# Kernel tuning notes

Hardware: AMD Instinct MI355X
Metric: run time of the kernel (lower is better)

## Reference

```python
import jax, jax.numpy as jnp
import numpy as np

B, T, C, H = 8, 2048, 1024, 128  # batch, seq (== block_size), n_embd, head_size


def setup_inputs() -> dict:
    key = jax.random.key(0)
    ks = jax.random.split(key, 4)
    s = 1.0 / np.sqrt(C)  # keep logits sane for softmax
    return {
        "embedded_data": jax.random.normal(ks[0], (B, T, C), dtype=jnp.float32),
        "Wq": jax.random.normal(ks[1], (C, H), dtype=jnp.float32) * s,
        "bq": jnp.zeros((H,), dtype=jnp.float32),
        "Wk": jax.random.normal(ks[2], (C, H), dtype=jnp.float32) * s,
        "bk": jnp.zeros((H,), dtype=jnp.float32),
        "Wv": jax.random.normal(ks[3], (C, H), dtype=jnp.float32) * s,
        "bv": jnp.zeros((H,), dtype=jnp.float32),
    }


def reference(embedded_data, Wq, bq, Wk, bk, Wv, bv):
    Bc, Tc, Cc = embedded_data.shape
    q = embedded_data @ Wq + bq                      # [B,T,H]
    k = embedded_data @ Wk + bk                      # [B,T,H]
    v = embedded_data @ Wv + bv                      # [B,T,H]
    # NOTE: source scales by C**-0.5 (input embed dim), not head_size**-0.5
    wei = jnp.einsum("bqh,bkh->bqk", q, k) * (Cc ** -0.5)  # [B,T,T]
    causal = jnp.tril(jnp.ones((Tc, Tc), dtype=bool))
    wei = jnp.where(causal, wei, -jnp.inf)
    wei = jax.nn.softmax(wei, axis=-1)
    # dropout(p=0.2) is identity in eval mode
    out = jnp.einsum("bqk,bkh->bqh", wei, v)         # [B,T,H]
    return out
```

## Files before the change

### kernel.cpp

```cpp
#include <hip/hip_runtime.h>
#include <cstdint>
#include <cstddef>

typedef __bf16 bf16x8 __attribute__((ext_vector_type(8)));
typedef float f32x4 __attribute__((ext_vector_type(4)));

#define B_ 8
#define T_ 2048
#define C_ 1024
#define H_ 128

#define QSC 0.045084220027780106f

__device__ __forceinline__ unsigned short f2bf(float f) {
    __bf16 h = (__bf16)f;
    return *(unsigned short*)&h;
}
__device__ __forceinline__ float bf2f(unsigned short u) {
    union { unsigned int i; float f; } x; x.i = ((unsigned int)u) << 16;
    return x.f;
}

__device__ __forceinline__ void gload16(void* lds, const void* g) {
    __builtin_amdgcn_global_load_lds(
        (const __attribute__((address_space(1))) unsigned int*)g,
        (__attribute__((address_space(3))) unsigned int*)lds, 16, 0, 0);
}

__global__ __launch_bounds__(256) void prep_w(
    const float* __restrict__ Wq, const float* __restrict__ Wk,
    const float* __restrict__ Wv, unsigned short* __restrict__ wt)
{
    int gid = blockIdx.x * 256 + threadIdx.x;
    int which = gid >> 14;
    int rem = gid & 16383;
    int n = rem >> 7;
    int kc = rem & 127;
    const float* W = which == 0 ? Wq : (which == 1 ? Wk : Wv);
    unsigned short tmp[8];
    #pragma unroll
    for (int i = 0; i < 8; ++i) tmp[i] = f2bf(W[(size_t)(kc * 8 + i) * H_ + n]);
    *(uint4*)&wt[((size_t)which * H_ + n) * C_ + kc * 8] = *(uint4*)tmp;
}

__global__ __launch_bounds__(384, 2) void proj_fused2(
    const float* __restrict__ x, const unsigned short* __restrict__ wt,
    const float* __restrict__ bq, const float* __restrict__ bk,
    const float* __restrict__ bv,
    unsigned short* __restrict__ qo, unsigned short* __restrict__ ko,
    unsigned short* __restrict__ vo)
{
    __shared__ float xs[2][64 * 64];
    __shared__ unsigned short ws2[2][384 * 64];

    const int tid = threadIdx.x;
    const int w = tid >> 6, l = tid & 63, gl = l >> 4, lc = l & 15;
    const int cb = w * 64;
    const int m0 = blockIdx.x * 64;

    f32x4 acc[4][4];
    #pragma unroll
    for (int im = 0; im < 4; ++im)
        #pragma unroll
        for (int jn = 0; jn < 4; ++jn) acc[im][jn] = f32x4{0.f, 0.f, 0.f, 0.f};

    auto stage = [&](int buf, int kc2) {
        const int kb = kc2 * 64;
        if (w < 4) {
            #pragma unroll
            for (int ji = 0; ji < 4; ++ji) {
                int slot = ji * 256 + tid;
                int r = slot >> 4, cs = slot & 15;
                gload16(&xs[buf][(ji * 256 + w * 64) * 4],
                        &x[(size_t)(m0 + r) * C_ + kb + ((cs ^ (r & 15)) * 4)]);
            }
        }
        #pragma unroll
        for (int ji = 0; ji < 8; ++ji) {
            int slot = ji * 384 + tid;
            int R = slot >> 3, cs = slot & 7;
            gload16(&ws2[buf][(ji * 384 + w * 64) * 8],
                    &wt[(size_t)R * C_ + kb + ((cs ^ (R & 7)) * 8)]);
        }
    };

    stage(0, 0);
    __syncthreads();

    int cur = 0;
    for (int kc = 0; kc < 16; ++kc) {
        if (kc < 15) stage(cur ^ 1, kc + 1);
        #pragma unroll
        for (int ks = 0; ks < 2; ++ks) {
            bf16x8 a[4], b[4];
            const int u0 = ks * 8 + gl * 2;
            #pragma unroll
            for (int im = 0; im < 4; ++im) {
                int row = im * 16 + lc;
                f32x4 lo = *(const f32x4*)&xs[cur][(row * 16 + (u0 ^ (row & 15))) * 4];
                f32x4 hi = *(const f32x4*)&xs[cur][(row * 16 + ((u0 + 1) ^ (row & 15))) * 4];
                bf16x8 af;
                af[0] = (__bf16)lo[0]; af[1] = (__bf16)lo[1];
                af[2] = (__bf16)lo[2]; af[3] = (__bf16)lo[3];
                af[4] = (__bf16)hi[0]; af[5] = (__bf16)hi[1];
                af[6] = (__bf16)hi[2]; af[7] = (__bf16)hi[3];
                a[im] = af;
            }
            #pragma unroll
            for (int jn = 0; jn < 4; ++jn) {
                int R = cb + jn * 16 + lc;
                b[jn] = *(const bf16x8*)&ws2[cur][(R * 8 + ((ks * 4 + gl) ^ (R & 7))) * 8];
            }
            #pragma unroll
            for (int im = 0; im < 4; ++im)
                #pragma unroll
                for (int jn = 0; jn < 4; ++jn)
                    acc[im][jn] = __builtin_amdgcn_mfma_f32_16x16x32_bf16(
                        a[im], b[jn], acc[im][jn], 0, 0, 0);
        }
        __syncthreads();
        cur ^= 1;
    }

    unsigned short* eb = (unsigned short*)&ws2[0][0];
    #pragma unroll
    for (int jn = 0; jn < 4; ++jn) {
        int n = cb + jn * 16 + lc;
        int wh = n >> 7, nl = n & 127;
        float bb = (wh == 0) ? bq[nl] : (wh == 1 ? bk[nl] : bv[nl]);
        float sc = (wh == 0) ? QSC : 1.0f;
        #pragma unroll
        for (int im = 0; im < 4; ++im)
            #pragma unroll
            for (int r = 0; r < 4; ++r) {
                int row = im * 16 + gl * 4 + r;
                eb[row * 392 + n] = f2bf((acc[im][jn][r] + bb) * sc);
            }
    }
    __syncthreads();

    const int bi = m0 >> 11, t0 = m0 & (T_ - 1);
    #pragma unroll
    for (int i = 0; i < 3; ++i) {
        int c = i * 384 + tid;
        if (c < 1024) {
            {
                int row = c >> 4, c16 = c & 15;
                *(uint4*)&qo[(size_t)(m0 + row) * H_ + c16 * 8] =
                    *(const uint4*)&eb[row * 392 + c16 * 8];
                *(uint4*)&ko[(size_t)(m0 + row) * H_ + c16 * 8] =
                    *(const uint4*)&eb[row * 392 + 128 + c16 * 8];
            }
            {
                int n = c >> 3, cc = c & 7;
                unsigned short tmp[8];
                #pragma unroll
                for (int ii = 0; ii < 8; ++ii)
                    tmp[ii] = eb[(cc * 8 + ii) * 392 + 256 + n];
                *(uint4*)&vo[((size_t)(bi * H_ + n)) * T_ + t0 + cc * 8] = *(uint4*)tmp;
            }
        }
    }
}

__device__ __forceinline__ int pasc(int qt) {
    int m = qt >> 2, j = qt & 3;
    return 2 * m * (m + 1) + j * (m + 1);
}

__global__ __launch_bounds__(256, 2) void attn_split7(
    const unsigned short* __restrict__ q,
    const unsigned short* __restrict__ k,
    const unsigned short* __restrict__ vT,
    float* __restrict__ out,
    unsigned short* __restrict__ Opart, float* __restrict__ lws)
{
    const int bb = blockIdx.x;
    const int jj = 143 - (int)blockIdx.y;
    int qt = 31;
    while (pasc(qt) > jj) --qt;
    const int c = jj - pasc(qt);
    const int nch = (qt >> 2) + 1;
    const int q0 = qt * 64;
    const int kstart = c * 256;
    const int kend = min(kstart + 256, q0 + 64);
    const int ntiles = (kend - kstart) >> 5;

    const unsigned short* qb = q  + (size_t)bb * T_ * H_;
    const unsigned short* kb = k  + (size_t)bb * T_ * H_;
    const unsigned short* vb = vT + (size_t)bb * H_ * T_;

    __shared__ unsigned short Ks[2][32 * 128];
    __shared__ unsigned short Vs[2][128 * 32];
    __shared__ unsigned short Ps[4][16 * 64];

    const int tid = threadIdx.x;
    const int w = tid >> 6, l = tid & 63, gl = l >> 4, lc = l & 15;
    const int rowbase = q0 + w * 16;

    bf16x8 aq[4];
    #pragma unroll
    for (int ds = 0; ds < 4; ++ds)
        aq[ds] = *(const bf16x8*)&qb[(size_t)(rowbase + lc) * H_ + ds * 32 + gl * 8];

    f32x4 o[8];
    #pragma unroll
    for (int jo = 0; jo < 8; ++jo) o[jo] = f32x4{0.f, 0.f, 0.f, 0.f};
    float l_acc[4];
    #pragma unroll
    for (int r = 0; r < 4; ++r) l_acc[r] = 0.f;

    auto stageK = [&](int buf, int t) {
        const int kv0 = kstart + t * 32;
        #pragma unroll
        for (int ji = 0; ji < 2; ++ji) {
            int slot = (w * 2 + ji) * 64 + l;
            int r = slot >> 4, cs = slot & 15;
            gload16(&Ks[buf][((w * 2 + ji) * 64) * 8],
                    &kb[(size_t)(kv0 + r) * H_ + ((cs ^ (r & 7)) * 8)]);
        }
    };
    auto stageV = [&](int buf, int t) {
        const int kv0 = kstart + t * 32;
        #pragma unroll
        for (int ji = 0; ji < 2; ++ji) {
            int slot = (w * 2 + ji) * 64 + l;
            int r = slot >> 2, cs = slot & 3;
            gload16(&Vs[buf][((w * 2 + ji) * 64) * 8],
                    &vb[(size_t)r * T_ + kv0 + ((cs ^ (r & 3)) * 8)]);
        }
    };

    stageK(0, 0);
    stageV(0, 0);
    __syncthreads();

    int cur = 0;
    for (int t = 0; t < ntiles; ++t) {
        if (t + 1 < ntiles) { stageK(cur ^ 1, t + 1); stageV(cur ^ 1, t + 1); }
        const int kv0 = kstart + t * 32;
        const bool active = kv0 < rowbase + 16;
        if (active) {
            f32x4 s[2];
            #pragma unroll
            for (int jk = 0; jk < 2; ++jk) s[jk] = f32x4{0.f, 0.f, 0.f, 0.f};
            #pragma unroll
            for (int ds = 0; ds < 4; ++ds) {
                #pragma unroll
                for (int jk = 0; jk < 2; ++jk) {
                    int row = jk * 16 + lc;
                    bf16x8 kf = *(const bf16x8*)&Ks[cur][(row * 16 + ((ds * 4 + gl) ^ (row & 7))) * 8];
                    s[jk] = __builtin_amdgcn_mfma_f32_16x16x32_bf16(aq[ds], kf, s[jk], 0, 0, 0);
                }
            }
            if (kv0 + 31 > rowbase) {
                #pragma unroll
                for (int jk = 0; jk < 2; ++jk)
                    #pragma unroll
                    for (int r = 0; r < 4; ++r)
                        if (kv0 + jk * 16 + lc > rowbase + gl * 4 + r) s[jk][r] = -1e30f;
            }
            #pragma unroll
            for (int jk = 0; jk < 2; ++jk)
                #pragma unroll
                for (int r = 0; r < 4; ++r) {
                    float p = exp2f(fminf(s[jk][r], 80.f));
                    s[jk][r] = p;
                    l_acc[r] += p;
                }
            #pragma unroll
            for (int jk = 0; jk < 2; ++jk)
                #pragma unroll
                for (int r = 0; r < 4; ++r) {
                    int row = gl * 4 + r;
                    Ps[w][(row * 64 + jk * 16 + lc) ^ ((row & 7) << 3)] = f2bf(s[jk][r]);
                }
            {
                bf16x8 pa = *(const bf16x8*)&Ps[w][(lc * 64 + gl * 8) ^ ((lc & 7) << 3)];
                #pragma unroll
                for (int jo = 0; jo < 8; ++jo) {
                    int d = jo * 16 + lc;
                    bf16x8 vf = *(const bf16x8*)&Vs[cur][(d * 4 + (gl ^ (d & 3))) * 8];
                    o[jo] = __builtin_amdgcn_mfma_f32_16x16x32_bf16(pa, vf, o[jo], 0, 0, 0);
                }
            }
        }
        __syncthreads();
        cur ^= 1;
    }

    #pragma unroll
    for (int off = 1; off < 16; off <<= 1)
        #pragma unroll
        for (int r = 0; r < 4; ++r)
            l_acc[r] += __shfl_xor(l_acc[r], off, 64);

    if (nch == 1) {
        float* ob = out + (size_t)bb * T_ * H_;
        float inv[4];
        #pragma unroll
        for (int r = 0; r < 4; ++r) inv[r] = 1.0f / l_acc[r];
        #pragma unroll
        for (int jo = 0; jo < 8; ++jo)
            #pragma unroll
            for (int r = 0; r < 4; ++r)
                ob[(size_t)(rowbase + gl * 4 + r) * H_ + jo * 16 + lc] = o[jo][r] * inv[r];
    } else {
        const int slot = bb * 140 + (pasc(qt) - 4 + c);
        unsigned short* op = Opart + (size_t)slot * 8192;
        #pragma unroll
        for (int jo = 0; jo < 8; ++jo)
            #pragma unroll
            for (int r = 0; r < 4; ++r)
                op[(w * 16 + gl * 4 + r) * 128 + jo * 16 + lc] = f2bf(o[jo][r]);
        if (lc == 0) {
            #pragma unroll
            for (int r = 0; r < 4; ++r)
                lws[slot * 64 + w * 16 + gl * 4 + r] = l_acc[r];
        }
    }
}

__global__ __launch_bounds__(256) void combine_kernel(
    const unsigned short* __restrict__ Opart, const float* __restrict__ lws,
    float* __restrict__ out)
{
    const int rowid = blockIdx.x * 4 + (threadIdx.x >> 6);
    const int lane = threadIdx.x & 63;
    const int bb = rowid / 1792;
    const int t = 256 + (rowid - bb * 1792);
    const int qt = t >> 6;
    const int m = qt >> 2;
    const int nch = m + 1;
    const int p0 = 2 * m * (m + 1) + (qt & 3) * (m + 1);
    const int base = bb * 140 + (p0 - 4);
    const int r64 = t & 63;

    float L = 0.f, a0 = 0.f, a1 = 0.f;
    #pragma unroll
    for (int c2 = 0; c2 < 8; ++c2)
        if (c2 < nch) {
            L += lws[(base + c2) * 64 + r64];
            ushort2 uv = *(const ushort2*)&Opart[(size_t)(base + c2) * 8192 + r64 * 128 + lane * 2];
            a0 += bf2f(uv.x); a1 += bf2f(uv.y);
        }
    const float invL = 1.0f / L;
    *(float2*)&out[((size_t)bb * T_ + t) * H_ + lane * 2] = make_float2(a0 * invL, a1 * invL);
}

__global__ __launch_bounds__(128) void attn_mono(
    const unsigned short* __restrict__ q,
    const unsigned short* __restrict__ k,
    const unsigned short* __restrict__ vT,
    float* __restrict__ out)
{
    const int qt = (gridDim.x - 1) - blockIdx.x;
    const int bb = blockIdx.y;
    const int q0 = qt * 32;
    const unsigned short* qb = q  + (size_t)bb * T_ * H_;
    const unsigned short* kb = k  + (size_t)bb * T_ * H_;
    const unsigned short* vb = vT + (size_t)bb * H_ * T_;

    __shared__ unsigned short Ps[2][16 * 64];

    const int tid = threadIdx.x;
    const int w = tid >> 6, l = tid & 63, gl = l >> 4, lc = l & 15;

    bf16x8 aq[4];
    #pragma unroll
    for (int ds = 0; ds < 4; ++ds)
        aq[ds] = *(const bf16x8*)&qb[(size_t)(q0 + w * 16 + lc) * H_ + ds * 32 + gl * 8];

    f32x4 o[8];
    #pragma unroll
    for (int jo = 0; jo < 8; ++jo) o[jo] = f32x4{0.f, 0.f, 0.f, 0.f};
    float m_run[4], l_run[4];
    #pragma unroll
    for (int r = 0; r < 4; ++r) { m_run[r] = -INFINITY; l_run[r] = 0.f; }

    const int nt = (q0 >> 6) + 1;
    for (int t = 0; t < nt; ++t) {
        const int kv0 = t * 64;
        f32x4 s[4];
        #pragma unroll
        for (int jk = 0; jk < 4; ++jk) s[jk] = f32x4{0.f, 0.f, 0.f, 0.f};
        #pragma unroll
        for (int ds = 0; ds < 4; ++ds)
            #pragma unroll
            for (int jk = 0; jk < 4; ++jk) {
                bf16x8 bf = *(const bf16x8*)&kb[(size_t)(kv0 + jk * 16 + lc) * H_ + ds * 32 + gl * 8];
                s[jk] = __builtin_amdgcn_mfma_f32_16x16x32_bf16(aq[ds], bf, s[jk], 0, 0, 0);
            }
        if (kv0 + 63 > q0) {
            const int rowg = q0 + w * 16 + gl * 4;
            #pragma unroll
            for (int jk = 0; jk < 4; ++jk)
                #pragma unroll
                for (int r = 0; r < 4; ++r)
                    if (kv0 + jk * 16 + lc > rowg + r) s[jk][r] = -1e30f;
        }
        float pm[4];
        #pragma unroll
        for (int r = 0; r < 4; ++r)
            pm[r] = fmaxf(fmaxf(s[0][r], s[1][r]), fmaxf(s[2][r], s[3][r]));
        #pragma unroll
        for (int off = 1; off < 16; off <<= 1)
            #pragma unroll
            for (int r = 0; r < 4; ++r)
                pm[r] = fmaxf(pm[r], __shfl_xor(pm[r], off, 64));
        float scl[4], rs[4];
        #pragma unroll
        for (int r = 0; r < 4; ++r) {
            float mn = fmaxf(m_run[r], pm[r]);
            scl[r] = exp2f(m_run[r] - mn);
            m_run[r] = mn;
            rs[r] = 0.f;
        }
        #pragma unroll
        for (int jk = 0; jk < 4; ++jk)
            #pragma unroll
            for (int r = 0; r < 4; ++r) {
                float p = exp2f(s[jk][r] - m_run[r]);
                s[jk][r] = p;
                rs[r] += p;
            }
        #pragma unroll
        for (int off = 1; off < 16; off <<= 1)
            #pragma unroll
            for (int r = 0; r < 4; ++r)
                rs[r] += __shfl_xor(rs[r], off, 64);
        #pragma unroll
        for (int r = 0; r < 4; ++r)
            l_run[r] = l_run[r] * scl[r] + rs[r];
        #pragma unroll
        for (int jo = 0; jo < 8; ++jo)
            #pragma unroll
            for (int r = 0; r < 4; ++r)
                o[jo][r] *= scl[r];
        #pragma unroll
        for (int jk = 0; jk < 4; ++jk)
            #pragma unroll
            for (int r = 0; r < 4; ++r) {
                int row = gl * 4 + r;
                Ps[w][(row * 64 + jk * 16 + lc) ^ ((row & 7) << 3)] = f2bf(s[jk][r]);
            }
        #pragma unroll
        for (int ks = 0; ks < 2; ++ks) {
            bf16x8 pa = *(const bf16x8*)&Ps[w][(lc * 64 + ks * 32 + gl * 8) ^ ((lc & 7) << 3)];
            #pragma unroll
            for (int jo = 0; jo < 8; ++jo) {
                bf16x8 bv_ = *(const bf16x8*)&vb[(size_t)(jo * 16 + lc) * T_ + kv0 + ks * 32 + gl * 8];
                o[jo] = __builtin_amdgcn_mfma_f32_16x16x32_bf16(pa, bv_, o[jo], 0, 0, 0);
            }
        }
    }
    float* ob = out + (size_t)bb * T_ * H_;
    #pragma unroll
    for (int jo = 0; jo < 8; ++jo)
        #pragma unroll
        for (int r = 0; r < 4; ++r)
            ob[(size_t)(q0 + w * 16 + gl * 4 + r) * H_ + jo * 16 + lc] = o[jo][r] / l_run[r];
}

extern "C" void kernel_launch(void* const* d_in, const int* in_sizes, int n_in,
                              void* d_out, int out_size, void* d_ws, size_t ws_size,
                              hipStream_t stream) {
    const float* x  = (const float*)d_in[0];
    const float* Wq = (const float*)d_in[1];
    const float* bq = (const float*)d_in[2];
    const float* Wk = (const float*)d_in[3];
    const float* bk = (const float*)d_in[4];
    const float* Wv = (const float*)d_in[5];
    const float* bv = (const float*)d_in[6];
    float* out = (float*)d_out;

    const size_t qkv = (size_t)B_ * T_ * H_;
    unsigned short* qws = (unsigned short*)d_ws;
    unsigned short* kws = qws + qkv;
    unsigned short* vws = kws + qkv;
    unsigned short* wtw = vws + qkv;
    const size_t base_bytes = (3 * qkv + (size_t)3 * H_ * C_) * 2;
    unsigned short* Opart = (unsigned short*)((char*)d_ws + base_bytes);
    float* lws = (float*)((char*)d_ws + base_bytes + (size_t)1120 * 8192 * 2);
    const size_t need = base_bytes + (size_t)1120 * 8192 * 2 + (size_t)1120 * 64 * 4;

    prep_w<<<dim3(192), 256, 0, stream>>>(Wq, Wk, Wv, wtw);
    proj_fused2<<<dim3(256), 384, 0, stream>>>(x, wtw, bq, bk, bv, qws, kws, vws);
    if (ws_size >= need) {
        attn_split7<<<dim3(8, 144), 256, 0, stream>>>(qws, kws, vws, out, Opart, lws);
        combine_kernel<<<dim3(3584), 256, 0, stream>>>(Opart, lws, out);
    } else {
        attn_mono<<<dim3(64, 8), 128, 0, stream>>>(qws, kws, vws, out);
    }
}
```

Baseline: 78.30 us.

## Widen QKV projection to 8 waves and deepen prefetch with vmcnt waits

The projection kernel moves from 6 to 8 waves per block, each wave now owning 48 output columns instead of 64, so per-wave accumulators shrink and all waves share the global-to-LDS staging. The double-buffer loop is restructured to issue stage kc+2 right after computing kc. It also waits with explicit vmcnt counts and raw s_barrier instead of a full __syncthreads, aiming to keep more loads in flight and cut barrier stalls. This relies on exact vmcnt bookkeeping and more threads per block, which may change occupancy.

```diff
diff --git a/kernel.cpp b/kernel.cpp
--- a/kernel.cpp
+++ b/kernel.cpp
@@ -43,7 +43,7 @@
     *(uint4*)&wt[((size_t)which * H_ + n) * C_ + kc * 8] = *(uint4*)tmp;
 }
 
-__global__ __launch_bounds__(384, 2) void proj_fused2(
+__global__ __launch_bounds__(512, 2) void proj_fused3(
     const float* __restrict__ x, const unsigned short* __restrict__ wt,
     const float* __restrict__ bq, const float* __restrict__ bk,
     const float* __restrict__ bv,
@@ -55,50 +55,50 @@
 
     const int tid = threadIdx.x;
     const int w = tid >> 6, l = tid & 63, gl = l >> 4, lc = l & 15;
-    const int cb = w * 64;
+    const int cb = w * 48;
     const int m0 = blockIdx.x * 64;
 
-    f32x4 acc[4][4];
+    f32x4 acc[4][3];
     #pragma unroll
     for (int im = 0; im < 4; ++im)
         #pragma unroll
-        for (int jn = 0; jn < 4; ++jn) acc[im][jn] = f32x4{0.f, 0.f, 0.f, 0.f};
+        for (int jn = 0; jn < 3; ++jn) acc[im][jn] = f32x4{0.f, 0.f, 0.f, 0.f};
 
     auto stage = [&](int buf, int kc2) {
         const int kb = kc2 * 64;
-        if (w < 4) {
-            #pragma unroll
-            for (int ji = 0; ji < 4; ++ji) {
-                int slot = ji * 256 + tid;
-                int r = slot >> 4, cs = slot & 15;
-                gload16(&xs[buf][(ji * 256 + w * 64) * 4],
-                        &x[(size_t)(m0 + r) * C_ + kb + ((cs ^ (r & 15)) * 4)]);
-            }
-        }
-        #pragma unroll
-        for (int ji = 0; ji < 8; ++ji) {
-            int slot = ji * 384 + tid;
+        #pragma unroll
+        for (int ji = 0; ji < 2; ++ji) {
+            int slot = ji * 512 + tid;
+            int r = slot >> 4, cs = slot & 15;
+            gload16(&xs[buf][(ji * 512 + w * 64) * 4],
+                    &x[(size_t)(m0 + r) * C_ + kb + ((cs ^ (r & 15)) * 4)]);
+        }
+        #pragma unroll
+        for (int ji = 0; ji < 6; ++ji) {
+            int slot = ji * 512 + tid;
             int R = slot >> 3, cs = slot & 7;
-            gload16(&ws2[buf][(ji * 384 + w * 64) * 8],
+            gload16(&ws2[buf][(ji * 512 + w * 64) * 8],
                     &wt[(size_t)R * C_ + kb + ((cs ^ (R & 7)) * 8)]);
         }
     };
 
     stage(0, 0);
-    __syncthreads();
-
-    int cur = 0;
+    stage(1, 1);
+    asm volatile("s_waitcnt vmcnt(8)" ::: "memory");
+    __builtin_amdgcn_sched_barrier(0);
+    __builtin_amdgcn_s_barrier();
+
     for (int kc = 0; kc < 16; ++kc) {
-        if (kc < 15) stage(cur ^ 1, kc + 1);
+        const int cur = kc & 1;
         #pragma unroll
         for (int ks = 0; ks < 2; ++ks) {
-            bf16x8 a[4], b[4];
+            bf16x8 a[4], b[3];
             const int u0 = ks * 8 + gl * 2;
             #pragma unroll
             for (int im = 0; im < 4; ++im) {
                 int row = im * 16 + lc;
-                f32x4 lo = *(const f32x4*)&xs[cur][(row * 16 + (u0 ^ (row & 15))) * 4];
-                f32x4 hi = *(const f32x4*)&xs[cur][(row * 16 + ((u0 + 1) ^ (row & 15))) * 4];
+                f32x4 lo = *(const f32x4*)&xs[cur][(row * 16 + (u0 ^ lc)) * 4];
+                f32x4 hi = *(const f32x4*)&xs[cur][(row * 16 + ((u0 + 1) ^ lc)) * 4];
                 bf16x8 af;
                 af[0] = (__bf16)lo[0]; af[1] = (__bf16)lo[1];
                 af[2] = (__bf16)lo[2]; af[3] = (__bf16)lo[3];
@@ -107,24 +107,33 @@
                 a[im] = af;
             }
             #pragma unroll
-            for (int jn = 0; jn < 4; ++jn) {
+            for (int jn = 0; jn < 3; ++jn) {
                 int R = cb + jn * 16 + lc;
-                b[jn] = *(const bf16x8*)&ws2[cur][(R * 8 + ((ks * 4 + gl) ^ (R & 7))) * 8];
+                b[jn] = *(const bf16x8*)&ws2[cur][(R * 8 + ((ks * 4 + gl) ^ (lc & 7))) * 8];
             }
             #pragma unroll
             for (int im = 0; im < 4; ++im)
                 #pragma unroll
-                for (int jn = 0; jn < 4; ++jn)
+                for (int jn = 0; jn < 3; ++jn)
                     acc[im][jn] = __builtin_amdgcn_mfma_f32_16x16x32_bf16(
                         a[im], b[jn], acc[im][jn], 0, 0, 0);
         }
-        __syncthreads();
-        cur ^= 1;
+        __builtin_amdgcn_s_barrier();
+        if (kc < 14) {
+            stage(cur, kc + 2);
+            asm volatile("s_waitcnt vmcnt(8)" ::: "memory");
+            __builtin_amdgcn_sched_barrier(0);
+            __builtin_amdgcn_s_barrier();
+        } else if (kc == 14) {
+            asm volatile("s_waitcnt vmcnt(0)" ::: "memory");
+            __builtin_amdgcn_sched_barrier(0);
+            __builtin_amdgcn_s_barrier();
+        }
     }
 
     unsigned short* eb = (unsigned short*)&ws2[0][0];
     #pragma unroll
-    for (int jn = 0; jn < 4; ++jn) {
+    for (int jn = 0; jn < 3; ++jn) {
         int n = cb + jn * 16 + lc;
         int wh = n >> 7, nl = n & 127;
         float bb = (wh == 0) ? bq[nl] : (wh == 1 ? bk[nl] : bv[nl]);
@@ -141,24 +150,22 @@
 
     const int bi = m0 >> 11, t0 = m0 & (T_ - 1);
     #pragma unroll
-    for (int i = 0; i < 3; ++i) {
-        int c = i * 384 + tid;
-        if (c < 1024) {
-            {
-                int row = c >> 4, c16 = c & 15;
-                *(uint4*)&qo[(size_t)(m0 + row) * H_ + c16 * 8] =
-                    *(const uint4*)&eb[row * 392 + c16 * 8];
-                *(uint4*)&ko[(size_t)(m0 + row) * H_ + c16 * 8] =
-                    *(const uint4*)&eb[row * 392 + 128 + c16 * 8];
-            }
-            {
-                int n = c >> 3, cc = c & 7;
-                unsigned short tmp[8];
-                #pragma unroll
-                for (int ii = 0; ii < 8; ++ii)
-                    tmp[ii] = eb[(cc * 8 + ii) * 392 + 256 + n];
-                *(uint4*)&vo[((size_t)(bi * H_ + n)) * T_ + t0 + cc * 8] = *(uint4*)tmp;
-            }
+    for (int i = 0; i < 2; ++i) {
+        int c = i * 512 + tid;
+        {
+            int row = c >> 4, c16 = c & 15;
+            *(uint4*)&qo[(size_t)(m0 + row) * H_ + c16 * 8] =
+                *(const uint4*)&eb[row * 392 + c16 * 8];
+            *(uint4*)&ko[(size_t)(m0 + row) * H_ + c16 * 8] =
+                *(const uint4*)&eb[row * 392 + 128 + c16 * 8];
+        }
+        {
+            int n = c >> 3, cc = c & 7;
+            unsigned short tmp[8];
+            #pragma unroll
+            for (int ii = 0; ii < 8; ++ii)
+                tmp[ii] = eb[(cc * 8 + ii) * 392 + 256 + n];
+            *(uint4*)&vo[((size_t)(bi * H_ + n)) * T_ + t0 + cc * 8] = *(uint4*)tmp;
         }
     }
 }
@@ -485,7 +492,7 @@
     const size_t need = base_bytes + (size_t)1120 * 8192 * 2 + (size_t)1120 * 64 * 4;
 
     prep_w<<<dim3(192), 256, 0, stream>>>(Wq, Wk, Wv, wtw);
-    proj_fused2<<<dim3(256), 384, 0, stream>>>(x, wtw, bq, bk, bv, qws, kws, vws);
+    proj_fused3<<<dim3(256), 512, 0, stream>>>(x, wtw, bq, bk, bv, qws, kws, vws);
     if (ws_size >= need) {
         attn_split7<<<dim3(8, 144), 256, 0, stream>>>(qws, kws, vws, out, Opart, lws);
         combine_kernel<<<dim3(3584), 256, 0, stream>>>(Opart, lws, out);
```

Result: faster. 72.31 us (-7.7%).
